# Kernel optimization log

Measured on AMD Instinct MI355X. Metric: run time of the kernel, lower is better.

## Reference

```python
import jax, jax.numpy as jnp
import numpy as np

SCALE = 16.0 / 8.0  # alpha / r

def setup_inputs() -> dict:
    key = jax.random.key(0)
    ks = jax.random.split(key, 6)
    B, S, IN_F, OUT_F, E, R = 4, 2048, 2048, 2048, 4, 8
    x = jax.random.normal(ks[0], (B, S, IN_F), dtype=jnp.float32)
    base_w = jax.random.normal(ks[1], (OUT_F, IN_F), dtype=jnp.float32) * (1.0 / np.sqrt(IN_F))
    base_b = jax.random.normal(ks[2], (OUT_F,), dtype=jnp.float32) * 0.02
    A = jax.random.normal(ks[3], (E, R, IN_F), dtype=jnp.float32) * (1.0 / np.sqrt(IN_F))
    Bm = jax.random.normal(ks[4], (E, OUT_F, R), dtype=jnp.float32) * 0.02
    router_w = jax.random.normal(ks[5], (E, IN_F), dtype=jnp.float32) * (1.0 / np.sqrt(IN_F))
    return {"x": x, "base_w": base_w, "base_b": base_b, "A": A, "B": Bm, "router_w": router_w}

def reference(x, base_w, base_b, A, B, router_w):
    # base linear: (B,S,out_f)
    base_out = jnp.einsum('bsi,oi->bso', x, base_w) + base_b
    # router + softmax gates over experts: (B,S,E)
    router_logits = jnp.einsum('bsi,ei->bse', x, router_w)
    gates = jax.nn.softmax(router_logits, axis=-1)
    # routing == 'weighted': use soft gates directly
    # LoRA: down-project to rank r per expert, then up-project
    proj_r = jnp.einsum('bsi,eri->bser', x, A)        # (B,S,E,r)
    lora_out = jnp.einsum('bser,eor->bseo', proj_r, B)  # (B,S,E,out_f)
    # gate-weighted sum over experts, scaled by alpha/r
    lora_mix = jnp.einsum('bseo,bse->bso', lora_out, gates * SCALE)
    return base_out + lora_mix
```

## Files before the change

### kernel.cpp

```cpp
#include <hip/hip_runtime.h>
#include <hip/hip_bf16.h>
#include <stdint.h>

#define M_ROWS 8192
#define KDIM   2048
#define NDIM   2048
#define SCALE_F 2.0f

typedef __attribute__((ext_vector_type(8))) short  bf16x8;
typedef __attribute__((ext_vector_type(4))) float  f32x4;
typedef __attribute__((ext_vector_type(4))) unsigned short u16x4;

__device__ __forceinline__ unsigned short f2bf(float f) {
    unsigned u = __float_as_uint(f);
    unsigned r = (u + 0x7fffu + ((u >> 16) & 1u)) >> 16;
    return (unsigned short)r;
}

#define GLOAD_LDS16(gptr, lptr) \
    __builtin_amdgcn_global_load_lds((const __attribute__((address_space(1))) void*)(gptr), \
                                     (__attribute__((address_space(3))) void*)(lptr), 16, 0, 0)

__global__ __launch_bounds__(256) void k_convert(
    const float* __restrict__ x,
    const float* __restrict__ bw,
    const float* __restrict__ A,
    const float* __restrict__ rw,
    const float* __restrict__ Bm,
    unsigned short* __restrict__ xb,
    unsigned short* __restrict__ wb,
    unsigned short* __restrict__ W36,
    unsigned short* __restrict__ Bc)
{
    const int t = blockIdx.x * 256 + threadIdx.x;
    const int nthr = gridDim.x * 256;

    const float4* x4 = (const float4*)x;
    for (int i = t; i < (M_ROWS * KDIM / 4); i += nthr) {
        float4 v = x4[i];
        u16x4 o = { f2bf(v.x), f2bf(v.y), f2bf(v.z), f2bf(v.w) };
        *(u16x4*)(xb + (size_t)i * 4) = o;
    }
    const float4* w4 = (const float4*)bw;
    for (int i = t; i < (NDIM * KDIM / 4); i += nthr) {
        float4 v = w4[i];
        u16x4 o = { f2bf(v.x), f2bf(v.y), f2bf(v.z), f2bf(v.w) };
        *(u16x4*)(wb + (size_t)i * 4) = o;
    }
    if (t < 48 * 2048) {
        int row = t >> 11, col = t & 2047;
        float v = (row < 32) ? A[row * 2048 + col]
                : (row < 36) ? rw[(row - 32) * 2048 + col] : 0.f;
        W36[t] = f2bf(v);
    }
    if (t < 4 * 2048 * 8) {
        int e = t >> 14, rem = t & 16383, o = rem >> 3, r = rem & 7;
        Bc[o * 32 + e * 8 + r] = f2bf(Bm[t]);
    }
}

__global__ __launch_bounds__(256) void k_proj(
    const unsigned short* __restrict__ xb,
    const unsigned short* __restrict__ W36,
    unsigned short* __restrict__ Wg)
{
    __shared__ unsigned short As[64 * 64];
    __shared__ unsigned short Ws[48 * 64];

    const int tid = threadIdx.x;
    const int l = tid & 63, w = tid >> 6;
    const int l15 = l & 15, l16h = l >> 4, l7 = l & 7;
    const int m0 = blockIdx.x * 64;
    const int st_col = ((l & 7) ^ (l >> 3)) * 8;

    f32x4 acc[3];
#pragma unroll
    for (int n = 0; n < 3; ++n) acc[n] = (f32x4){0.f, 0.f, 0.f, 0.f};

    for (int kt = 0; kt < KDIM / 64; ++kt) {
        const int k0 = kt * 64;
        {
            unsigned short* lp = As + w * 1024;
            const unsigned short* gp = xb + (size_t)(m0 + w * 16 + (l >> 3)) * KDIM + k0 + st_col;
            GLOAD_LDS16(gp, lp);
            GLOAD_LDS16(gp + (size_t)8 * KDIM, lp + 512);
        }
        if (w < 3) {
            unsigned short* lp = Ws + w * 1024;
            const unsigned short* gp = W36 + (size_t)(w * 16 + (l >> 3)) * KDIM + k0 + st_col;
            GLOAD_LDS16(gp, lp);
            GLOAD_LDS16(gp + (size_t)8 * KDIM, lp + 512);
        }
        __syncthreads();

#pragma unroll
        for (int kk = 0; kk < 2; ++kk) {
            const int arow = w * 16 + l15;
            bf16x8 a = *(const bf16x8*)&As[arow * 64 + (((kk * 4 + l16h) ^ l7) << 3)];
#pragma unroll
            for (int n = 0; n < 3; ++n) {
                const int brow = n * 16 + l15;
                bf16x8 b = *(const bf16x8*)&Ws[brow * 64 + (((kk * 4 + l16h) ^ l7) << 3)];
                acc[n] = __builtin_amdgcn_mfma_f32_16x16x32_bf16(a, b, acc[n], 0, 0, 0);
            }
        }
        __syncthreads();
    }

#pragma unroll
    for (int j = 0; j < 4; ++j) {
        const int base = l & 48;
        float lg0 = __shfl(acc[2][j], base + 0);
        float lg1 = __shfl(acc[2][j], base + 1);
        float lg2 = __shfl(acc[2][j], base + 2);
        float lg3 = __shfl(acc[2][j], base + 3);
        float mx = fmaxf(fmaxf(lg0, lg1), fmaxf(lg2, lg3));
        float e0 = __expf(lg0 - mx), e1 = __expf(lg1 - mx);
        float e2 = __expf(lg2 - mx), e3 = __expf(lg3 - mx);
        float inv = SCALE_F / (e0 + e1 + e2 + e3);
        float g0 = e0 * inv, g1 = e1 * inv, g2 = e2 * inv, g3 = e3 * inv;

        const int row = m0 + w * 16 + (l >> 4) * 4 + j;
#pragma unroll
        for (int n = 0; n < 2; ++n) {
            const int cn = n * 16 + l15;
            const int e = cn >> 3;
            float g = (e == 0) ? g0 : (e == 1) ? g1 : (e == 2) ? g2 : g3;
            Wg[(size_t)row * 32 + cn] = f2bf(g * acc[n][j]);
        }
    }
}

#define GPHASE(JB, Q, STAGE_STMT, CKPT_STMT) do {                              \
    bf16x8 afr_[4][2];                                                         \
    _Pragma("unroll") for (int mi = 0; mi < 4; ++mi) {                         \
      const int row_ = wr * 64 + mi * 16 + l15;                                \
      const int ab_ = (JB) * 16384 + ((Q) & 1) * 8192 + row_ * 64;             \
      _Pragma("unroll") for (int kk = 0; kk < 2; ++kk)                         \
        afr_[mi][kk] = *(const bf16x8*)&S[ab_ + (((kk * 4 + l16h) ^ l7) << 3)];\
    }                                                                          \
    if (((Q) & 1) == 0) {                                                      \
      _Pragma("unroll") for (int ni = 0; ni < 2; ++ni) {                       \
        const int row_ = wc * 32 + ni * 16 + l15;                              \
        const int bb_ = 32768 + (JB) * 16384 + ((Q) >> 1) * 8192 + row_ * 64;  \
        _Pragma("unroll") for (int kk = 0; kk < 2; ++kk)                       \
          bfr[ni][kk] = *(const bf16x8*)&S[bb_ + (((kk * 4 + l16h) ^ l7) << 3)];\
      }                                                                        \
    }                                                                          \
    STAGE_STMT                                                                 \
    CKPT_STMT                                                                  \
    __builtin_amdgcn_s_barrier();                                              \
    __builtin_amdgcn_s_setprio(1);                                             \
    _Pragma("unroll") for (int mi = 0; mi < 4; ++mi)                           \
      _Pragma("unroll") for (int ni = 0; ni < 2; ++ni)                         \
        _Pragma("unroll") for (int kk = 0; kk < 2; ++kk)                       \
          acc[((Q) & 1) * 4 + mi][((Q) >> 1) * 2 + ni] =                       \
            __builtin_amdgcn_mfma_f32_16x16x32_bf16(afr_[mi][kk], bfr[ni][kk], \
              acc[((Q) & 1) * 4 + mi][((Q) >> 1) * 2 + ni], 0, 0, 0);          \
    __builtin_amdgcn_s_setprio(0);                                             \
    __builtin_amdgcn_s_barrier();                                              \
  } while (0)

__global__ __launch_bounds__(512, 2) void k_gemm(
    const unsigned short* __restrict__ xb,
    const unsigned short* __restrict__ wb,
    const unsigned short* __restrict__ Wg,
    const unsigned short* __restrict__ Bc,
    const float* __restrict__ bias,
    float* __restrict__ out)
{
    extern __shared__ unsigned short S[];

    const int tid = threadIdx.x;
    const int l = tid & 63, w = tid >> 6;
    const int l15 = l & 15, l16h = l >> 4, l7 = l & 7;
    const int wr = w >> 2, wc = w & 3;

    const int bid = blockIdx.x;
    const int tile = (bid & 7) * 32 + (bid >> 3);
    const int mt = tile >> 3, nt = tile & 7;
    const int m0 = mt * 256, n0 = nt * 256;

    const int st_row = w * 8 + (l >> 3);
    const int st_col = ((l & 7) ^ (l >> 3)) * 8;

    auto stageA = [&](int t, int h) {
        unsigned short* lp = S + ((t & 1) * 16384 + h * 8192 + w * 512);
        const unsigned short* gp = xb + (size_t)(m0 + h * 128 + st_row) * KDIM + t * 64 + st_col;
        GLOAD_LDS16(gp, lp);
        GLOAD_LDS16(gp + (size_t)64 * KDIM, lp + 4096);
    };
    auto stageB = [&](int t, int h) {
        unsigned short* lp = S + (32768 + (t & 1) * 16384 + h * 8192 + w * 512);
        const unsigned short* gp = wb + (size_t)(n0 + h * 128 + st_row) * KDIM + t * 64 + st_col;
        GLOAD_LDS16(gp, lp);
        GLOAD_LDS16(gp + (size_t)64 * KDIM, lp + 4096);
    };

    f32x4 acc[8][4];
#pragma unroll
    for (int m = 0; m < 8; ++m)
#pragma unroll
        for (int n = 0; n < 4; ++n)
            acc[m][n] = (f32x4){0.f, 0.f, 0.f, 0.f};
    bf16x8 bfr[2][2];

    stageA(0, 0); stageA(0, 1); stageB(0, 0); stageB(0, 1);
    stageB(1, 0); stageA(1, 0);
    asm volatile("s_waitcnt vmcnt(4)" ::: "memory");
    __builtin_amdgcn_s_barrier();

#pragma unroll 2
    for (int j = 0; j < 32; ++j) {
        const int jb = j & 1;
        GPHASE(jb, 0, { if (j < 31) stageB(j + 1, 1); }, );
        GPHASE(jb, 1, { if (j < 31) stageA(j + 1, 1); }, );
        GPHASE(jb, 2, { if (j < 30) stageB(j + 2, 0); }, );
        GPHASE(jb, 3, { if (j < 30) stageA(j + 2, 0); },
               { if (j < 30) { asm volatile("s_waitcnt vmcnt(4)" ::: "memory"); }
                 else        { asm volatile("s_waitcnt vmcnt(0)" ::: "memory"); } });
    }

    {
        const int lw_row = w * 16 + (l >> 2);
        const int lw_col = (l & 3) * 8;
        unsigned short* lpA = S + w * 512;
        const unsigned short* gpA = Wg + (size_t)(m0 + lw_row) * 32 + lw_col;
        GLOAD_LDS16(gpA, lpA);
        GLOAD_LDS16(gpA + (size_t)128 * 32, lpA + 4096);
        unsigned short* lpB = S + 32768 + w * 512;
        const unsigned short* gpB = Bc + (size_t)(n0 + lw_row) * 32 + lw_col;
        GLOAD_LDS16(gpB, lpB);
        GLOAD_LDS16(gpB + (size_t)128 * 32, lpB + 4096);
    }
    asm volatile("s_waitcnt vmcnt(0)" ::: "memory");
    __builtin_amdgcn_s_barrier();

#pragma unroll
    for (int m = 0; m < 8; ++m) {
        bf16x8 af = *(const bf16x8*)&S[((m >> 2) * 128 + wr * 64 + (m & 3) * 16 + l15) * 32 + l16h * 8];
#pragma unroll
        for (int n = 0; n < 4; ++n) {
            bf16x8 bf = *(const bf16x8*)&S[32768 + ((n >> 1) * 128 + wc * 32 + (n & 1) * 16 + l15) * 32 + l16h * 8];
            acc[m][n] = __builtin_amdgcn_mfma_f32_16x16x32_bf16(af, bf, acc[m][n], 0, 0, 0);
        }
    }

#pragma unroll
    for (int n = 0; n < 4; ++n) {
        const int cn = n0 + (n >> 1) * 128 + wc * 32 + (n & 1) * 16 + l15;
        const float bv = bias[cn];
#pragma unroll
        for (int m = 0; m < 8; ++m) {
            const int rm = m0 + (m >> 2) * 128 + wr * 64 + (m & 3) * 16 + l16h * 4;
#pragma unroll
            for (int jj = 0; jj < 4; ++jj)
                out[(size_t)(rm + jj) * NDIM + cn] = acc[m][n][jj] + bv;
        }
    }
}

extern "C" void kernel_launch(void* const* d_in, const int* in_sizes, int n_in,
                              void* d_out, int out_size, void* d_ws, size_t ws_size,
                              hipStream_t stream) {
    const float* x      = (const float*)d_in[0];
    const float* base_w = (const float*)d_in[1];
    const float* base_b = (const float*)d_in[2];
    const float* A      = (const float*)d_in[3];
    const float* Bm     = (const float*)d_in[4];
    const float* rw     = (const float*)d_in[5];
    float* out = (float*)d_out;

    char* ws = (char*)d_ws;
    unsigned short* xb  = (unsigned short*)(ws);
    unsigned short* wb  = (unsigned short*)(ws + 33554432);
    unsigned short* W36 = (unsigned short*)(ws + 33554432 + 8388608);
    unsigned short* Wg  = (unsigned short*)(ws + 33554432 + 8388608 + 196608);
    unsigned short* Bc  = (unsigned short*)(ws + 33554432 + 8388608 + 196608 + 524288);

    k_convert<<<dim3(2048), dim3(256), 0,      stream>>>(x, base_w, A, rw, Bm, xb, wb, W36, Bc);
    k_proj   <<<dim3(128),  dim3(256), 0,      stream>>>(xb, W36, Wg);
    k_gemm   <<<dim3(256),  dim3(512), 131072, stream>>>(xb, wb, Wg, Bc, base_b, out);
}
```

Before: 222.1 us.

## Widen conversion stores, split projection into single-wave blocks, restructure GEMM fragment reuse

The conversion kernel now processes eight floats per thread and writes 16-byte bf16 vectors, including the W36 and Bc packing. The projection kernel drops its LDS staging and barriers and uses 512 single-wave blocks that load MFMA fragments straight from global memory, which spreads work across more CUs. The main GEMM keeps A fragments across two phases and caches both B halves, which cuts redundant LDS reads, and it precomputes LDS and global offsets. The gain is bounded because the large GEMM dominates total time, and direct global loads in the projection kernel may be less coalesced.

```diff
diff --git a/kernel.cpp b/kernel.cpp
--- a/kernel.cpp
+++ b/kernel.cpp
@@ -9,7 +9,7 @@
 
 typedef __attribute__((ext_vector_type(8))) short  bf16x8;
 typedef __attribute__((ext_vector_type(4))) float  f32x4;
-typedef __attribute__((ext_vector_type(4))) unsigned short u16x4;
+typedef __attribute__((ext_vector_type(8))) unsigned short u16x8;
 
 __device__ __forceinline__ unsigned short f2bf(float f) {
     unsigned u = __float_as_uint(f);
@@ -35,76 +35,73 @@
     const int t = blockIdx.x * 256 + threadIdx.x;
     const int nthr = gridDim.x * 256;
 
-    const float4* x4 = (const float4*)x;
-    for (int i = t; i < (M_ROWS * KDIM / 4); i += nthr) {
-        float4 v = x4[i];
-        u16x4 o = { f2bf(v.x), f2bf(v.y), f2bf(v.z), f2bf(v.w) };
-        *(u16x4*)(xb + (size_t)i * 4) = o;
-    }
-    const float4* w4 = (const float4*)bw;
-    for (int i = t; i < (NDIM * KDIM / 4); i += nthr) {
-        float4 v = w4[i];
-        u16x4 o = { f2bf(v.x), f2bf(v.y), f2bf(v.z), f2bf(v.w) };
-        *(u16x4*)(wb + (size_t)i * 4) = o;
-    }
-    if (t < 48 * 2048) {
-        int row = t >> 11, col = t & 2047;
-        float v = (row < 32) ? A[row * 2048 + col]
-                : (row < 36) ? rw[(row - 32) * 2048 + col] : 0.f;
-        W36[t] = f2bf(v);
-    }
-    if (t < 4 * 2048 * 8) {
-        int e = t >> 14, rem = t & 16383, o = rem >> 3, r = rem & 7;
-        Bc[o * 32 + e * 8 + r] = f2bf(Bm[t]);
-    }
-}
-
-__global__ __launch_bounds__(256) void k_proj(
+    for (int i = t; i < (M_ROWS * KDIM / 8); i += nthr) {
+        float4 v0 = *(const float4*)(x + (size_t)i * 8);
+        float4 v1 = *(const float4*)(x + (size_t)i * 8 + 4);
+        u16x8 o = { f2bf(v0.x), f2bf(v0.y), f2bf(v0.z), f2bf(v0.w),
+                    f2bf(v1.x), f2bf(v1.y), f2bf(v1.z), f2bf(v1.w) };
+        *(u16x8*)(xb + (size_t)i * 8) = o;
+    }
+    for (int i = t; i < (NDIM * KDIM / 8); i += nthr) {
+        float4 v0 = *(const float4*)(bw + (size_t)i * 8);
+        float4 v1 = *(const float4*)(bw + (size_t)i * 8 + 4);
+        u16x8 o = { f2bf(v0.x), f2bf(v0.y), f2bf(v0.z), f2bf(v0.w),
+                    f2bf(v1.x), f2bf(v1.y), f2bf(v1.z), f2bf(v1.w) };
+        *(u16x8*)(wb + (size_t)i * 8) = o;
+    }
+    if (t < 48 * 2048 / 8) {
+        const int row = (t * 8) >> 11, col = (t * 8) & 2047;
+        u16x8 o;
+        if (row < 36) {
+            const float* src = (row < 32) ? (A + (size_t)row * 2048 + col)
+                                          : (rw + (size_t)(row - 32) * 2048 + col);
+            float4 v0 = *(const float4*)(src);
+            float4 v1 = *(const float4*)(src + 4);
+            o = (u16x8){ f2bf(v0.x), f2bf(v0.y), f2bf(v0.z), f2bf(v0.w),
+                         f2bf(v1.x), f2bf(v1.y), f2bf(v1.z), f2bf(v1.w) };
+        } else {
+            o = (u16x8){0, 0, 0, 0, 0, 0, 0, 0};
+        }
+        *(u16x8*)(W36 + (size_t)t * 8) = o;
+    }
+    if (t < 4 * 2048) {
+        const int e = t >> 11, o = t & 2047;
+        const float* src = Bm + ((size_t)e * 2048 + o) * 8;
+        float4 v0 = *(const float4*)(src);
+        float4 v1 = *(const float4*)(src + 4);
+        u16x8 ov = { f2bf(v0.x), f2bf(v0.y), f2bf(v0.z), f2bf(v0.w),
+                     f2bf(v1.x), f2bf(v1.y), f2bf(v1.z), f2bf(v1.w) };
+        *(u16x8*)(Bc + (size_t)o * 32 + e * 8) = ov;
+    }
+}
+
+__global__ __launch_bounds__(64) void k_proj(
     const unsigned short* __restrict__ xb,
     const unsigned short* __restrict__ W36,
     unsigned short* __restrict__ Wg)
 {
-    __shared__ unsigned short As[64 * 64];
-    __shared__ unsigned short Ws[48 * 64];
-
-    const int tid = threadIdx.x;
-    const int l = tid & 63, w = tid >> 6;
-    const int l15 = l & 15, l16h = l >> 4, l7 = l & 7;
-    const int m0 = blockIdx.x * 64;
-    const int st_col = ((l & 7) ^ (l >> 3)) * 8;
+    const int l = threadIdx.x;
+    const int l15 = l & 15, l16h = l >> 4;
+    const int row0 = blockIdx.x * 16;
+
+    const unsigned short* pa = xb + (size_t)(row0 + l15) * KDIM + l16h * 8;
+    const unsigned short* pb0 = W36 + (size_t)(0 * 16 + l15) * KDIM + l16h * 8;
+    const unsigned short* pb1 = W36 + (size_t)(1 * 16 + l15) * KDIM + l16h * 8;
+    const unsigned short* pb2 = W36 + (size_t)(2 * 16 + l15) * KDIM + l16h * 8;
 
     f32x4 acc[3];
 #pragma unroll
     for (int n = 0; n < 3; ++n) acc[n] = (f32x4){0.f, 0.f, 0.f, 0.f};
 
-    for (int kt = 0; kt < KDIM / 64; ++kt) {
-        const int k0 = kt * 64;
-        {
-            unsigned short* lp = As + w * 1024;
-            const unsigned short* gp = xb + (size_t)(m0 + w * 16 + (l >> 3)) * KDIM + k0 + st_col;
-            GLOAD_LDS16(gp, lp);
-            GLOAD_LDS16(gp + (size_t)8 * KDIM, lp + 512);
-        }
-        if (w < 3) {
-            unsigned short* lp = Ws + w * 1024;
-            const unsigned short* gp = W36 + (size_t)(w * 16 + (l >> 3)) * KDIM + k0 + st_col;
-            GLOAD_LDS16(gp, lp);
-            GLOAD_LDS16(gp + (size_t)8 * KDIM, lp + 512);
-        }
-        __syncthreads();
-
-#pragma unroll
-        for (int kk = 0; kk < 2; ++kk) {
-            const int arow = w * 16 + l15;
-            bf16x8 a = *(const bf16x8*)&As[arow * 64 + (((kk * 4 + l16h) ^ l7) << 3)];
-#pragma unroll
-            for (int n = 0; n < 3; ++n) {
-                const int brow = n * 16 + l15;
-                bf16x8 b = *(const bf16x8*)&Ws[brow * 64 + (((kk * 4 + l16h) ^ l7) << 3)];
-                acc[n] = __builtin_amdgcn_mfma_f32_16x16x32_bf16(a, b, acc[n], 0, 0, 0);
-            }
-        }
-        __syncthreads();
+#pragma unroll 4
+    for (int kt = 0; kt < KDIM / 32; ++kt) {
+        bf16x8 a = *(const bf16x8*)(pa + kt * 32);
+        bf16x8 b0 = *(const bf16x8*)(pb0 + kt * 32);
+        bf16x8 b1 = *(const bf16x8*)(pb1 + kt * 32);
+        bf16x8 b2 = *(const bf16x8*)(pb2 + kt * 32);
+        acc[0] = __builtin_amdgcn_mfma_f32_16x16x32_bf16(a, b0, acc[0], 0, 0, 0);
+        acc[1] = __builtin_amdgcn_mfma_f32_16x16x32_bf16(a, b1, acc[1], 0, 0, 0);
+        acc[2] = __builtin_amdgcn_mfma_f32_16x16x32_bf16(a, b2, acc[2], 0, 0, 0);
     }
 
 #pragma unroll
@@ -120,7 +117,7 @@
         float inv = SCALE_F / (e0 + e1 + e2 + e3);
         float g0 = e0 * inv, g1 = e1 * inv, g2 = e2 * inv, g3 = e3 * inv;
 
-        const int row = m0 + w * 16 + (l >> 4) * 4 + j;
+        const int row = row0 + l16h * 4 + j;
 #pragma unroll
         for (int n = 0; n < 2; ++n) {
             const int cn = n * 16 + l15;
@@ -131,20 +128,17 @@
     }
 }
 
-#define GPHASE(JB, Q, STAGE_STMT, CKPT_STMT) do {                              \
-    bf16x8 afr_[4][2];                                                         \
-    _Pragma("unroll") for (int mi = 0; mi < 4; ++mi) {                         \
-      const int row_ = wr * 64 + mi * 16 + l15;                                \
-      const int ab_ = (JB) * 16384 + ((Q) & 1) * 8192 + row_ * 64;             \
-      _Pragma("unroll") for (int kk = 0; kk < 2; ++kk)                         \
-        afr_[mi][kk] = *(const bf16x8*)&S[ab_ + (((kk * 4 + l16h) ^ l7) << 3)];\
+#define PH(JB, AH, BH, DO_ARD, DO_BRD, STAGE_STMT, CKPT_STMT) do {             \
+    if (DO_ARD) {                                                              \
+      _Pragma("unroll") for (int mi = 0; mi < 4; ++mi) {                       \
+        afr[mi][0] = *(const bf16x8*)&S[(JB)*16384 + (AH)*8192 + mi*1024 + aoff0]; \
+        afr[mi][1] = *(const bf16x8*)&S[(JB)*16384 + (AH)*8192 + mi*1024 + aoff1]; \
+      }                                                                        \
     }                                                                          \
-    if (((Q) & 1) == 0) {                                                      \
+    if (DO_BRD) {                                                              \
       _Pragma("unroll") for (int ni = 0; ni < 2; ++ni) {                       \
-        const int row_ = wc * 32 + ni * 16 + l15;                              \
-        const int bb_ = 32768 + (JB) * 16384 + ((Q) >> 1) * 8192 + row_ * 64;  \
-        _Pragma("unroll") for (int kk = 0; kk < 2; ++kk)                       \
-          bfr[ni][kk] = *(const bf16x8*)&S[bb_ + (((kk * 4 + l16h) ^ l7) << 3)];\
+        bfr[BH][ni][0] = *(const bf16x8*)&Sb[(JB)*16384 + (BH)*8192 + ni*1024 + boff0]; \
+        bfr[BH][ni][1] = *(const bf16x8*)&Sb[(JB)*16384 + (BH)*8192 + ni*1024 + boff1]; \
       }                                                                        \
     }                                                                          \
     STAGE_STMT                                                                 \
@@ -152,11 +146,12 @@
     __builtin_amdgcn_s_barrier();                                              \
     __builtin_amdgcn_s_setprio(1);                                             \
     _Pragma("unroll") for (int mi = 0; mi < 4; ++mi)                           \
-      _Pragma("unroll") for (int ni = 0; ni < 2; ++ni)                         \
-        _Pragma("unroll") for (int kk = 0; kk < 2; ++kk)                       \
-          acc[((Q) & 1) * 4 + mi][((Q) >> 1) * 2 + ni] =                       \
-            __builtin_amdgcn_mfma_f32_16x16x32_bf16(afr_[mi][kk], bfr[ni][kk], \
-              acc[((Q) & 1) * 4 + mi][((Q) >> 1) * 2 + ni], 0, 0, 0);          \
+      _Pragma("unroll") for (int ni = 0; ni < 2; ++ni) {                       \
+        acc[(AH)*4+mi][(BH)*2+ni] = __builtin_amdgcn_mfma_f32_16x16x32_bf16(   \
+            afr[mi][0], bfr[BH][ni][0], acc[(AH)*4+mi][(BH)*2+ni], 0, 0, 0);   \
+        acc[(AH)*4+mi][(BH)*2+ni] = __builtin_amdgcn_mfma_f32_16x16x32_bf16(   \
+            afr[mi][1], bfr[BH][ni][1], acc[(AH)*4+mi][(BH)*2+ni], 0, 0, 0);   \
+      }                                                                        \
     __builtin_amdgcn_s_setprio(0);                                             \
     __builtin_amdgcn_s_barrier();                                              \
   } while (0)
@@ -170,6 +165,7 @@
     float* __restrict__ out)
 {
     extern __shared__ unsigned short S[];
+    unsigned short* Sb = S + 32768;
 
     const int tid = threadIdx.x;
     const int l = tid & 63, w = tid >> 6;
@@ -181,18 +177,26 @@
     const int mt = tile >> 3, nt = tile & 7;
     const int m0 = mt * 256, n0 = nt * 256;
 
+    const int aoff0 = (wr * 64 + l15) * 64 + ((l16h ^ l7) << 3);
+    const int aoff1 = (wr * 64 + l15) * 64 + (((4 + l16h) ^ l7) << 3);
+    const int boff0 = (wc * 32 + l15) * 64 + ((l16h ^ l7) << 3);
+    const int boff1 = (wc * 32 + l15) * 64 + (((4 + l16h) ^ l7) << 3);
+
     const int st_row = w * 8 + (l >> 3);
     const int st_col = ((l & 7) ^ (l >> 3)) * 8;
+    const unsigned short* gA0 = xb + (size_t)(m0 + st_row) * KDIM + st_col;
+    const unsigned short* gB0 = wb + (size_t)(n0 + st_row) * KDIM + st_col;
+    const int sw = w * 512;
 
     auto stageA = [&](int t, int h) {
-        unsigned short* lp = S + ((t & 1) * 16384 + h * 8192 + w * 512);
-        const unsigned short* gp = xb + (size_t)(m0 + h * 128 + st_row) * KDIM + t * 64 + st_col;
+        unsigned short* lp = S + ((t & 1) * 16384 + h * 8192 + sw);
+        const unsigned short* gp = gA0 + (size_t)h * 128 * KDIM + t * 64;
         GLOAD_LDS16(gp, lp);
         GLOAD_LDS16(gp + (size_t)64 * KDIM, lp + 4096);
     };
     auto stageB = [&](int t, int h) {
-        unsigned short* lp = S + (32768 + (t & 1) * 16384 + h * 8192 + w * 512);
-        const unsigned short* gp = wb + (size_t)(n0 + h * 128 + st_row) * KDIM + t * 64 + st_col;
+        unsigned short* lp = Sb + ((t & 1) * 16384 + h * 8192 + sw);
+        const unsigned short* gp = gB0 + (size_t)h * 128 * KDIM + t * 64;
         GLOAD_LDS16(gp, lp);
         GLOAD_LDS16(gp + (size_t)64 * KDIM, lp + 4096);
     };
@@ -203,7 +207,8 @@
 #pragma unroll
         for (int n = 0; n < 4; ++n)
             acc[m][n] = (f32x4){0.f, 0.f, 0.f, 0.f};
-    bf16x8 bfr[2][2];
+    bf16x8 afr[4][2];
+    bf16x8 bfr[2][2][2];
 
     stageA(0, 0); stageA(0, 1); stageB(0, 0); stageB(0, 1);
     stageB(1, 0); stageA(1, 0);
@@ -213,22 +218,22 @@
 #pragma unroll 2
     for (int j = 0; j < 32; ++j) {
         const int jb = j & 1;
-        GPHASE(jb, 0, { if (j < 31) stageB(j + 1, 1); }, );
-        GPHASE(jb, 1, { if (j < 31) stageA(j + 1, 1); }, );
-        GPHASE(jb, 2, { if (j < 30) stageB(j + 2, 0); }, );
-        GPHASE(jb, 3, { if (j < 30) stageA(j + 2, 0); },
-               { if (j < 30) { asm volatile("s_waitcnt vmcnt(4)" ::: "memory"); }
-                 else        { asm volatile("s_waitcnt vmcnt(0)" ::: "memory"); } });
+        PH(jb, 0, 0, 1, 1, { if (j < 31) stageB(j + 1, 1); }, );
+        PH(jb, 0, 1, 0, 1, { if (j < 31) stageA(j + 1, 1); }, );
+        PH(jb, 1, 0, 1, 0, { if (j < 30) stageB(j + 2, 0); }, );
+        PH(jb, 1, 1, 0, 0, { if (j < 30) stageA(j + 2, 0); },
+           { if (j < 30) { asm volatile("s_waitcnt vmcnt(4)" ::: "memory"); }
+             else        { asm volatile("s_waitcnt vmcnt(0)" ::: "memory"); } });
     }
 
     {
         const int lw_row = w * 16 + (l >> 2);
         const int lw_col = (l & 3) * 8;
-        unsigned short* lpA = S + w * 512;
+        unsigned short* lpA = S + sw;
         const unsigned short* gpA = Wg + (size_t)(m0 + lw_row) * 32 + lw_col;
         GLOAD_LDS16(gpA, lpA);
         GLOAD_LDS16(gpA + (size_t)128 * 32, lpA + 4096);
-        unsigned short* lpB = S + 32768 + w * 512;
+        unsigned short* lpB = Sb + sw;
         const unsigned short* gpB = Bc + (size_t)(n0 + lw_row) * 32 + lw_col;
         GLOAD_LDS16(gpB, lpB);
         GLOAD_LDS16(gpB + (size_t)128 * 32, lpB + 4096);
@@ -241,7 +246,7 @@
         bf16x8 af = *(const bf16x8*)&S[((m >> 2) * 128 + wr * 64 + (m & 3) * 16 + l15) * 32 + l16h * 8];
 #pragma unroll
         for (int n = 0; n < 4; ++n) {
-            bf16x8 bf = *(const bf16x8*)&S[32768 + ((n >> 1) * 128 + wc * 32 + (n & 1) * 16 + l15) * 32 + l16h * 8];
+            bf16x8 bf = *(const bf16x8*)&Sb[((n >> 1) * 128 + wc * 32 + (n & 1) * 16 + l15) * 32 + l16h * 8];
             acc[m][n] = __builtin_amdgcn_mfma_f32_16x16x32_bf16(af, bf, acc[m][n], 0, 0, 0);
         }
     }
@@ -279,6 +284,6 @@
     unsigned short* Bc  = (unsigned short*)(ws + 33554432 + 8388608 + 196608 + 524288);
 
     k_convert<<<dim3(2048), dim3(256), 0,      stream>>>(x, base_w, A, rw, Bm, xb, wb, W36, Bc);
-    k_proj   <<<dim3(128),  dim3(256), 0,      stream>>>(xb, W36, Wg);
+    k_proj   <<<dim3(512),  dim3(64),  0,      stream>>>(xb, W36, Wg);
     k_gemm   <<<dim3(256),  dim3(512), 131072, stream>>>(xb, wb, Wg, Bc, base_b, out);
 }
```

Measured after the change: 218.9 us. Within noise of the previous version (-1.4%).
